# Performance work log

Measured on AMD Instinct MI355X. Metric: run time of the kernel, lower is better.

## Reference

```python
import jax, jax.numpy as jnp
import numpy as np

N = 12288
E = 393216
IN_DIM = 128
HID = 64
QK = 32
K_HOPS = 2


def setup_inputs() -> dict:
    key = jax.random.key(0)
    ks = jax.random.split(key, 12)
    s = lambda k, shp, fan: jax.random.normal(k, shp, jnp.float32) / np.sqrt(fan)
    return {
        "x_train": jax.random.normal(ks[0], (N, IN_DIM), jnp.float32),
        "x_ori": jax.random.normal(ks[1], (N, IN_DIM), jnp.float32),
        "edge_index": jax.random.randint(ks[2], (2, E), 0, N, jnp.int64),
        "mask": jnp.zeros((N,), jnp.bool_),
        "W1": s(ks[3], (IN_DIM, HID), IN_DIM), "b1": jnp.zeros((HID,), jnp.float32),
        "W2": s(ks[4], (HID, HID), HID),      "b2": jnp.zeros((HID,), jnp.float32),
        "Wq": s(ks[5], (HID, QK), HID),       "bq": jnp.zeros((QK,), jnp.float32),
        "Wk": s(ks[6], (HID, QK), HID),       "bk": jnp.zeros((QK,), jnp.float32),
        "Wv": s(ks[7], (HID, HID), HID),      "bv": jnp.zeros((HID,), jnp.float32),
        "Wdx": s(ks[8], (HID, IN_DIM), HID),  "bdx": jnp.zeros((IN_DIM,), jnp.float32),
    }


def reference(x_train, x_ori, edge_index, mask,
              W1, b1, W2, b2, Wq, bq, Wk, bk, Wv, bv, Wdx, bdx):
    n = x_train.shape[0]
    row, col = edge_index[0], edge_index[1]

    # shared MLP: linear -> relu -> linear2 -> relu
    enc = lambda x: jax.nn.relu(jax.nn.relu(x @ W1 + b1) @ W2 + b2)
    h_ori = enc(x_ori)      # [N, HID]
    h_train = enc(x_train)  # [N, HID]

    # degree of source nodes, D^{-1/2}
    deg = jax.ops.segment_sum(jnp.ones_like(row, jnp.float32), row, num_segments=n)
    d_invsqrt = jnp.clip(deg, 1.0, None) ** -0.5  # [N]
    d_invsqrt = d_invsqrt[:, None]

    def lap(x):
        h = x * d_invsqrt
        out = jax.ops.segment_sum(h[row], col, num_segments=n)
        return x - out * d_invsqrt

    a_feat = 2.0 * h_train - lap(h_train)  # low-pass: 2I - L_sym
    stack = [a_feat]
    x = h_train
    for _ in range(K_HOPS):  # dropout inert in eval mode
        x = lap(x)
        stack.append(x)
    L = jnp.stack(stack, axis=1)  # [N, K+1, HID]

    # attention with global mean-pooled query over h_ori[~mask]
    w = (~mask).astype(jnp.float32)
    q_nodes = h_ori @ Wq + bq                              # [N, QK]
    q_global = (q_nodes * w[:, None]).sum(0) / jnp.clip(w.sum(), 1.0, None)  # [QK]
    keys = L @ Wk + bk   # [N, K+1, QK]
    vals = L @ Wv + bv   # [N, K+1, HID]
    scale = 1.0 / np.sqrt(HID)  # scale uses D = keys feature dim BEFORE projection
    scores = jnp.einsum('q,nkq->nk', q_global, keys) * scale
    A = jax.nn.softmax(scores, axis=-1)          # [N, K+1]
    z = jnp.einsum('nk,nkd->nd', A, vals)        # [N, HID]

    x_hat = z @ Wdx + bdx   # [N, IN_DIM]
    adj_hat = z @ z.T       # [N, N]
    return x_hat, adj_hat
```

## Files before the change

### kernel.cpp

```cpp
#include <hip/hip_runtime.h>
#include <hip/hip_bf16.h>

constexpr int N_  = 12288;
constexpr int E_  = 393216;
constexpr int IND = 128;
constexpr int HID = 64;
constexpr int QKD = 32;
constexpr int CAP = 96;

typedef __attribute__((ext_vector_type(4))) float f4raw;
typedef __attribute__((ext_vector_type(8))) __bf16 bf16x8;
typedef __attribute__((ext_vector_type(4))) __bf16 bf16x4;
typedef __attribute__((ext_vector_type(16))) float f32x16;

__device__ inline bf16x8 lds_read_bf8(const char* base, int row, int k) {
  int off = (row * 128 + k * 2) ^ ((row & 7) << 4);
  uint4 u = *(const uint4*)(base + off);
  union { uint4 u; bf16x8 v; } c; c.u = u; return c.v;
}
__device__ inline void lds_write_bf(char* base, int row, int col, __bf16 v) {
  int off = (row * 128 + col * 2) ^ ((row & 7) << 4);
  *(__bf16*)(base + off) = v;
}

__global__ __launch_bounds__(256) void prep_graph_kernel(
    const float* __restrict__ xo, const float* __restrict__ xt,
    const int* __restrict__ row, const int* __restrict__ col,
    const float* __restrict__ W1, const float* __restrict__ W2,
    const float* __restrict__ Wv, const float* __restrict__ Wdx,
    __bf16* __restrict__ xb, __bf16* __restrict__ W1T, __bf16* __restrict__ W2T,
    __bf16* __restrict__ WvT, __bf16* __restrict__ WdxT,
    int* degRow, int* cntCol, int* __restrict__ csrRow) {
  int b = blockIdx.x, tid = threadIdx.x;
  if (b < 384) {
    int e0 = (b * 256 + tid) * 4;
    int4 r4 = *(const int4*)(row + e0);
    atomicAdd(&degRow[r4.x], 1);
    atomicAdd(&degRow[r4.y], 1);
    atomicAdd(&degRow[r4.z], 1);
    atomicAdd(&degRow[r4.w], 1);
  } else if (b < 768) {
    int e0 = ((b - 384) * 256 + tid) * 4;
    int4 r4 = *(const int4*)(row + e0);
    int4 c4 = *(const int4*)(col + e0);
    int p;
    p = atomicAdd(&cntCol[c4.x], 1); csrRow[c4.x * CAP + p] = r4.x;
    p = atomicAdd(&cntCol[c4.y], 1); csrRow[c4.y * CAP + p] = r4.y;
    p = atomicAdd(&cntCol[c4.z], 1); csrRow[c4.z * CAP + p] = r4.z;
    p = atomicAdd(&cntCol[c4.w], 1); csrRow[c4.w * CAP + p] = r4.w;
  } else if (b < 2304) {
    size_t base = (size_t)(b - 768) * 2048 + (size_t)tid * 8;
    const size_t half = (size_t)N_ * IND;
    const float* src = (base < half) ? (xo + base) : (xt + (base - half));
    f4raw v0 = *(const f4raw*)(src);
    f4raw v1 = *(const f4raw*)(src + 4);
    bf16x8 o;
    o[0] = (__bf16)v0.x; o[1] = (__bf16)v0.y; o[2] = (__bf16)v0.z; o[3] = (__bf16)v0.w;
    o[4] = (__bf16)v1.x; o[5] = (__bf16)v1.y; o[6] = (__bf16)v1.z; o[7] = (__bf16)v1.w;
    *(bf16x8*)(xb + base) = o;
  } else if (b == 2304) {
    for (int e = tid; e < IND * HID; e += 256) {
      int c = e >> 7, k = e & 127;
      W1T[e] = (__bf16)W1[k * HID + c];
    }
  } else if (b == 2305) {
    for (int e = tid; e < HID * HID; e += 256) {
      int c = e >> 6, k = e & 63;
      W2T[e] = (__bf16)W2[k * HID + c];
    }
  } else if (b == 2306) {
    for (int e = tid; e < HID * HID; e += 256) {
      int c = e >> 6, k = e & 63;
      WvT[e] = (__bf16)Wv[k * HID + c];
    }
  } else {
    for (int e = tid; e < HID * IND; e += 256) {
      int c = e >> 6, k = e & 63;
      WdxT[e] = (__bf16)Wdx[k * IND + c];
    }
  }
}

__global__ __launch_bounds__(256) void enc_dinv_kernel(
    const __bf16* __restrict__ xb,
    const __bf16* __restrict__ W1T, const float* __restrict__ b1,
    const __bf16* __restrict__ W2T, const float* __restrict__ b2,
    const int* __restrict__ degRow, const unsigned char* __restrict__ mask,
    float* __restrict__ h_tr, float* __restrict__ dinv, float* __restrict__ gsum) {
  __shared__ __align__(16) char h1s[2][32 * 128];
  __shared__ float wls[64];
  int b = blockIdx.x, tid = threadIdx.x;
  if (b >= 384) {
    int i0 = ((b - 384) * 256 + tid) * 4;
    int4 dg = *(const int4*)(degRow + i0);
    f4raw o = {rsqrtf((float)max(dg.x, 1)), rsqrtf((float)max(dg.y, 1)),
               rsqrtf((float)max(dg.z, 1)), rsqrtf((float)max(dg.w, 1))};
    *(f4raw*)(dinv + i0) = o;
    return;
  }
  bool ori = b < 192;
  int row0 = (ori ? b : b - 192) * 64;
  const __bf16* xrow = xb + (ori ? (size_t)0 : (size_t)N_ * IND) + (size_t)row0 * IND;
  if (ori && tid < 64) wls[tid] = mask[row0 + tid] ? 0.f : 1.f;
  int wave = tid >> 6, lane = tid & 63;
  int p = wave >> 1, w2 = wave & 1;
  int lr = lane & 31, hi = lane >> 5;
  int colc = w2 * 32 + lr;
  f32x16 acc = (f32x16)(0.f);
  const __bf16* wcol = W1T + (size_t)colc * IND + hi * 8;
  const __bf16* arow = xrow + (size_t)(p * 32 + lr) * IND + hi * 8;
#pragma unroll
  for (int kk = 0; kk < 8; ++kk) {
    bf16x8 a = *(const bf16x8*)(arow + kk * 16);
    bf16x8 bq = *(const bf16x8*)(wcol + kk * 16);
    acc = __builtin_amdgcn_mfma_f32_32x32x16_bf16(a, bq, acc, 0, 0, 0);
  }
  float b1l = b1[colc];
#pragma unroll
  for (int reg = 0; reg < 16; ++reg) {
    int rr = (reg & 3) + 8 * (reg >> 2) + 4 * hi;
    float v = fmaxf(acc[reg] + b1l, 0.f);
    lds_write_bf(h1s[p], rr, colc, (__bf16)v);
  }
  __syncthreads();
  f32x16 acc2 = (f32x16)(0.f);
  const __bf16* wcol2 = W2T + (size_t)colc * HID + hi * 8;
#pragma unroll
  for (int kk = 0; kk < 4; ++kk) {
    bf16x8 a = lds_read_bf8(h1s[p], lr, kk * 16 + hi * 8);
    bf16x8 bq = *(const bf16x8*)(wcol2 + kk * 16);
    acc2 = __builtin_amdgcn_mfma_f32_32x32x16_bf16(a, bq, acc2, 0, 0, 0);
  }
  float b2l = b2[colc];
  if (ori) {
    float part = 0.f;
#pragma unroll
    for (int reg = 0; reg < 16; ++reg) {
      int rr = (reg & 3) + 8 * (reg >> 2) + 4 * hi;
      float v = fmaxf(acc2[reg] + b2l, 0.f);
      part = fmaf(wls[p * 32 + rr], v, part);
    }
    atomicAdd(&gsum[colc], part);
    if (tid == 0) {
      float wl = 0.f;
      for (int r = 0; r < 64; ++r) wl += wls[r];
      atomicAdd(&gsum[64], wl);
    }
  } else {
#pragma unroll
    for (int reg = 0; reg < 16; ++reg) {
      int rr = (reg & 3) + 8 * (reg >> 2) + 4 * hi;
      float v = fmaxf(acc2[reg] + b2l, 0.f);
      h_tr[(size_t)(row0 + p * 32 + rr) * HID + colc] = v;
    }
  }
}

__global__ __launch_bounds__(256) void lap1_kernel(
    const float* __restrict__ h, const float* __restrict__ dinv,
    const int* __restrict__ cnt, const int* __restrict__ csrRow,
    float* __restrict__ lap1d) {
  int lane = threadIdx.x & 63, wv = threadIdx.x >> 6;
  int g = lane >> 4, t = lane & 15;
  int c = blockIdx.x * 16 + wv * 4 + g;
  int s0 = c * CAP, s1 = s0 + cnt[c];
  f4raw a0 = (f4raw)(0.f), a1 = (f4raw)(0.f);
  int i = s0;
  for (; i + 1 < s1; i += 2) {
    int r0 = csrRow[i], r1 = csrRow[i + 1];
    a0 += (*(const f4raw*)(h + (size_t)r0 * HID + t * 4)) * dinv[r0];
    a1 += (*(const f4raw*)(h + (size_t)r1 * HID + t * 4)) * dinv[r1];
  }
  if (i < s1) {
    int r0 = csrRow[i];
    a0 += (*(const f4raw*)(h + (size_t)r0 * HID + t * 4)) * dinv[r0];
  }
  float d = dinv[c];
  size_t idx = (size_t)c * HID + t * 4;
  f4raw hc = *(const f4raw*)(h + idx);
  *(f4raw*)(lap1d + idx) = (hc - (a0 + a1) * d) * d;
}

__global__ __launch_bounds__(256) void lap2_attnz_xhat_kernel(
    const float* __restrict__ h, const float* __restrict__ lap1d,
    const float* __restrict__ dinv,
    const int* __restrict__ cnt, const int* __restrict__ csrRow,
    const float* __restrict__ gsum,
    const float* __restrict__ Wq, const float* __restrict__ bq,
    const float* __restrict__ Wk, const float* __restrict__ bk,
    const __bf16* __restrict__ WvT, const float* __restrict__ bv,
    const __bf16* __restrict__ WdxT, const float* __restrict__ bdx,
    float* __restrict__ xhat, __bf16* __restrict__ zb) {
  __shared__ float l2s[32][68];
  __shared__ __align__(16) char zps[32 * 128];
  __shared__ __align__(16) char zsl[32 * 128];
  __shared__ float qg[QKD];
  __shared__ float kqs[72];
  int tid = threadIdx.x;
  int row0 = blockIdx.x * 32;
  float wsum = gsum[64];
  if (tid < QKD) {
    float inv = 1.0f / fmaxf(wsum, 1.0f);
    float a = bq[tid] * wsum;
    for (int d0 = 0; d0 < HID; ++d0) a = fmaf(gsum[d0], Wq[d0 * QKD + tid], a);
    qg[tid] = a * inv;
  }
  int grp = tid >> 4, t = tid & 15;
#pragma unroll
  for (int it = 0; it < 2; ++it) {
    int r = grp + 16 * it;
    int c = row0 + r;
    int s0 = c * CAP, s1 = s0 + cnt[c];
    f4raw a0 = (f4raw)(0.f), a1 = (f4raw)(0.f);
    int i = s0;
    for (; i + 1 < s1; i += 2) {
      int r0 = csrRow[i], r1 = csrRow[i + 1];
      a0 += *(const f4raw*)(lap1d + (size_t)r0 * HID + t * 4);
      a1 += *(const f4raw*)(lap1d + (size_t)r1 * HID + t * 4);
    }
    if (i < s1) {
      int r0 = csrRow[i];
      a0 += *(const f4raw*)(lap1d + (size_t)r0 * HID + t * 4);
    }
    float d = dinv[c];
    float rd = 1.0f / d;
    f4raw lv = *(const f4raw*)(lap1d + (size_t)c * HID + t * 4);
    *(f4raw*)&l2s[r][t * 4] = lv * rd - (a0 + a1) * d;
  }
  __syncthreads();
  if (tid < 64) {
    float a = 0.f;
    for (int q = 0; q < QKD; ++q) a = fmaf(Wk[tid * QKD + q], qg[q], a);
    kqs[tid] = a * 0.125f;
  } else if (tid == 64) {
    float sb = 0.f;
    for (int q = 0; q < QKD; ++q) sb = fmaf(bk[q], qg[q], sb);
    kqs[64] = sb * 0.125f;
  }
  __syncthreads();
  f4raw kq4 = *(const f4raw*)(&kqs[t * 4]);
  float sbias = kqs[64];
#pragma unroll
  for (int it = 0; it < 2; ++it) {
    int r = grp + 16 * it;
    int c = row0 + r;
    size_t idx = (size_t)c * HID + t * 4;
    float d = dinv[c];
    float rd = 1.0f / d;
    f4raw hv = *(const f4raw*)(h + idx);
    f4raw v1 = *(const f4raw*)(lap1d + idx) * rd;
    f4raw v2 = *(const f4raw*)&l2s[r][t * 4];
    f4raw av = 2.f * hv - v1;
    float s0 = av.x * kq4.x + av.y * kq4.y + av.z * kq4.z + av.w * kq4.w;
    float s1 = v1.x * kq4.x + v1.y * kq4.y + v1.z * kq4.z + v1.w * kq4.w;
    float s2 = v2.x * kq4.x + v2.y * kq4.y + v2.z * kq4.z + v2.w * kq4.w;
#pragma unroll
    for (int o = 1; o < 16; o <<= 1) {
      s0 += __shfl_xor(s0, o);
      s1 += __shfl_xor(s1, o);
      s2 += __shfl_xor(s2, o);
    }
    s0 += sbias; s1 += sbias; s2 += sbias;
    float m = fmaxf(s0, fmaxf(s1, s2));
    float e0 = __expf(s0 - m), e1 = __expf(s1 - m), e2 = __expf(s2 - m);
    float is = 1.f / (e0 + e1 + e2);
    f4raw zp = (e0 * av + e1 * v1 + e2 * v2) * is;
    bf16x4 z4;
    z4[0] = (__bf16)zp.x; z4[1] = (__bf16)zp.y; z4[2] = (__bf16)zp.z; z4[3] = (__bf16)zp.w;
    int off = (r * 128 + t * 8) ^ ((r & 7) << 4);
    *(bf16x4*)(zps + off) = z4;
  }
  __syncthreads();
  int wave = tid >> 6, lane = tid & 63;
  int lr = lane & 31, hi = lane >> 5;
  if (wave < 2) {
    int col = wave * 32 + lr;
    f32x16 accz = (f32x16)(0.f);
    const __bf16* wv = WvT + (size_t)col * HID + hi * 8;
#pragma unroll
    for (int kk = 0; kk < 4; ++kk) {
      bf16x8 a = lds_read_bf8(zps, lr, kk * 16 + hi * 8);
      bf16x8 bq = *(const bf16x8*)(wv + kk * 16);
      accz = __builtin_amdgcn_mfma_f32_32x32x16_bf16(a, bq, accz, 0, 0, 0);
    }
    float bvl = bv[col];
#pragma unroll
    for (int reg = 0; reg < 16; ++reg) {
      int rr = (reg & 3) + 8 * (reg >> 2) + 4 * hi;
      __bf16 vb = (__bf16)(accz[reg] + bvl);
      zb[(size_t)(row0 + rr) * HID + col] = vb;
      lds_write_bf(zsl, rr, col, vb);
    }
  }
  __syncthreads();
  {
    int c0 = wave * 32 + lr;
    f32x16 acx = (f32x16)(0.f);
    const __bf16* wd = WdxT + (size_t)c0 * HID + hi * 8;
#pragma unroll
    for (int kk = 0; kk < 4; ++kk) {
      bf16x8 a = lds_read_bf8(zsl, lr, kk * 16 + hi * 8);
      bf16x8 bq = *(const bf16x8*)(wd + kk * 16);
      acx = __builtin_amdgcn_mfma_f32_32x32x16_bf16(a, bq, acx, 0, 0, 0);
    }
    float bdl = bdx[c0];
#pragma unroll
    for (int reg = 0; reg < 16; ++reg) {
      int rr = (reg & 3) + 8 * (reg >> 2) + 4 * hi;
      xhat[(size_t)(row0 + rr) * IND + c0] = acx[reg] + bdl;
    }
  }
}

__global__ __launch_bounds__(256) void adj_mfma_kernel(
    const __bf16* __restrict__ z, float* __restrict__ out) {
  int tid = threadIdx.x;
  int wave = tid >> 6, lane = tid & 63;
  int wr = wave >> 1, wc = wave & 1;
  int rb = blockIdx.y, cb = blockIdx.x;
  int lr = lane & 31, hi = lane >> 5;

  size_t arow0 = (size_t)(rb * 128 + wr * 64 + lr) * HID;
  size_t arow1 = arow0 + (size_t)32 * HID;
  size_t brow0 = (size_t)(cb * 128 + wc * 64 + lr) * HID;
  size_t brow1 = brow0 + (size_t)32 * HID;
  int kbase = hi * 8;

  f32x16 acc00 = (f32x16)(0.f), acc01 = (f32x16)(0.f);
  f32x16 acc10 = (f32x16)(0.f), acc11 = (f32x16)(0.f);

#pragma unroll
  for (int kk = 0; kk < 4; ++kk) {
    int k0 = kk * 16 + kbase;
    bf16x8 a0 = *(const bf16x8*)(z + arow0 + k0);
    bf16x8 a1 = *(const bf16x8*)(z + arow1 + k0);
    bf16x8 b0 = *(const bf16x8*)(z + brow0 + k0);
    bf16x8 b1 = *(const bf16x8*)(z + brow1 + k0);
    acc00 = __builtin_amdgcn_mfma_f32_32x32x16_bf16(a0, b0, acc00, 0, 0, 0);
    acc01 = __builtin_amdgcn_mfma_f32_32x32x16_bf16(a0, b1, acc01, 0, 0, 0);
    acc10 = __builtin_amdgcn_mfma_f32_32x32x16_bf16(a1, b0, acc10, 0, 0, 0);
    acc11 = __builtin_amdgcn_mfma_f32_32x32x16_bf16(a1, b1, acc11, 0, 0, 0);
  }

  int colb = cb * 128 + wc * 64 + lr;
  int rowb = rb * 128 + wr * 64 + 4 * hi;
#pragma unroll
  for (int reg = 0; reg < 16; ++reg) {
    int rr = (reg & 3) + 8 * (reg >> 2);
    size_t r0 = (size_t)(rowb + rr);
    __builtin_nontemporal_store(acc00[reg], out + r0 * N_ + colb);
    __builtin_nontemporal_store(acc01[reg], out + r0 * N_ + colb + 32);
    __builtin_nontemporal_store(acc10[reg], out + (r0 + 32) * N_ + colb);
    __builtin_nontemporal_store(acc11[reg], out + (r0 + 32) * N_ + colb + 32);
  }
}

extern "C" void kernel_launch(void* const* d_in, const int* in_sizes, int n_in,
                              void* d_out, int out_size, void* d_ws, size_t ws_size,
                              hipStream_t stream) {
  const float* x_train = (const float*)d_in[0];
  const float* x_ori   = (const float*)d_in[1];
  const int*   ei      = (const int*)d_in[2];
  const unsigned char* mask = (const unsigned char*)d_in[3];
  const float* W1  = (const float*)d_in[4];
  const float* b1  = (const float*)d_in[5];
  const float* W2  = (const float*)d_in[6];
  const float* b2  = (const float*)d_in[7];
  const float* Wq  = (const float*)d_in[8];
  const float* bq  = (const float*)d_in[9];
  const float* Wk  = (const float*)d_in[10];
  const float* bk  = (const float*)d_in[11];
  const float* Wv  = (const float*)d_in[12];
  const float* bv  = (const float*)d_in[13];
  const float* Wdx = (const float*)d_in[14];
  const float* bdx = (const float*)d_in[15];

  char* ws = (char*)d_ws;
  size_t o = 0;
  auto alloc = [&](size_t bytes) -> void* {
    void* p = ws + o;
    o += (bytes + 255) & ~(size_t)255;
    return p;
  };
  __bf16* xb    = (__bf16*)alloc((size_t)2 * N_ * IND * 2);
  __bf16* W1T   = (__bf16*)alloc((size_t)IND * HID * 2);
  __bf16* W2T   = (__bf16*)alloc((size_t)HID * HID * 2);
  __bf16* WvT   = (__bf16*)alloc((size_t)HID * HID * 2);
  __bf16* WdxT  = (__bf16*)alloc((size_t)HID * IND * 2);
  float* h_tr   = (float*)alloc((size_t)N_ * HID * 4);
  float* lap1d  = (float*)alloc((size_t)N_ * HID * 4);
  __bf16* zb    = (__bf16*)alloc((size_t)N_ * HID * 2);
  float* dinv   = (float*)alloc((size_t)N_ * 4);
  int*   csrRow = (int*)alloc((size_t)N_ * CAP * 4);
  int*   zero0  = (int*)alloc((size_t)(2 * N_ + 65) * 4);
  int*   degRow = zero0;
  int*   cntCol = zero0 + N_;
  float* gsum   = (float*)(zero0 + 2 * N_);

  const int* row = ei;
  const int* col = ei + E_;

  (void)hipMemsetAsync(zero0, 0, (size_t)(2 * N_ + 65) * 4, stream);

  prep_graph_kernel<<<2308, 256, 0, stream>>>(x_ori, x_train, row, col,
                                              W1, W2, Wv, Wdx,
                                              xb, W1T, W2T, WvT, WdxT,
                                              degRow, cntCol, csrRow);
  enc_dinv_kernel<<<396, 256, 0, stream>>>(xb, W1T, b1, W2T, b2, degRow, mask,
                                           h_tr, dinv, gsum);
  lap1_kernel<<<N_ / 16, 256, 0, stream>>>(h_tr, dinv, cntCol, csrRow, lap1d);

  float* outp = (float*)d_out;
  lap2_attnz_xhat_kernel<<<N_ / 32, 256, 0, stream>>>(h_tr, lap1d, dinv,
                                                      cntCol, csrRow, gsum,
                                                      Wq, bq, Wk, bk, WvT, bv,
                                                      WdxT, bdx, outp, zb);
  adj_mfma_kernel<<<dim3(96, 96), 256, 0, stream>>>(zb, outp + (size_t)N_ * IND);
}
```

Measured before the change: 254.2 us.

## Fold Wv into Wdx so x_hat runs in parallel with z projection

Precomputes the combined weight Wv·Wdx and bias bv·Wdx+bdx in the prep kernel. x_hat can then be computed directly from the attention-pooled features, on waves 2-3, at the same time as waves 0-1 compute z. This removes a serial MFMA stage, an LDS buffer and a barrier from the fused kernel. It also unrolls the CSR gather loops in both Laplacian kernels to four accumulators for more memory-level parallelism. The fused weight is rounded to bf16 once, which changes rounding slightly, and the 8192-element weight product runs serially on a single prep block.

```diff
diff --git a/kernel.cpp b/kernel.cpp
--- a/kernel.cpp
+++ b/kernel.cpp
@@ -28,8 +28,9 @@
     const int* __restrict__ row, const int* __restrict__ col,
     const float* __restrict__ W1, const float* __restrict__ W2,
     const float* __restrict__ Wv, const float* __restrict__ Wdx,
+    const float* __restrict__ bv, const float* __restrict__ bdx,
     __bf16* __restrict__ xb, __bf16* __restrict__ W1T, __bf16* __restrict__ W2T,
-    __bf16* __restrict__ WvT, __bf16* __restrict__ WdxT,
+    __bf16* __restrict__ WvT, __bf16* __restrict__ WvdxT, float* __restrict__ bvdx,
     int* degRow, int* cntCol, int* __restrict__ csrRow) {
   int b = blockIdx.x, tid = threadIdx.x;
   if (b < 384) {
@@ -74,9 +75,16 @@
       WvT[e] = (__bf16)Wv[k * HID + c];
     }
   } else {
-    for (int e = tid; e < HID * IND; e += 256) {
+    for (int e = tid; e < IND * HID; e += 256) {
       int c = e >> 6, k = e & 63;
-      WdxT[e] = (__bf16)Wdx[k * IND + c];
+      float a = 0.f;
+      for (int j = 0; j < HID; ++j) a = fmaf(Wv[k * HID + j], Wdx[j * IND + c], a);
+      WvdxT[e] = (__bf16)a;
+    }
+    if (tid < IND) {
+      float a = bdx[tid];
+      for (int j = 0; j < HID; ++j) a = fmaf(bv[j], Wdx[j * IND + tid], a);
+      bvdx[tid] = a;
     }
   }
 }
@@ -164,21 +172,23 @@
   int g = lane >> 4, t = lane & 15;
   int c = blockIdx.x * 16 + wv * 4 + g;
   int s0 = c * CAP, s1 = s0 + cnt[c];
-  f4raw a0 = (f4raw)(0.f), a1 = (f4raw)(0.f);
+  f4raw a0 = (f4raw)(0.f), a1 = (f4raw)(0.f), a2 = (f4raw)(0.f), a3 = (f4raw)(0.f);
   int i = s0;
-  for (; i + 1 < s1; i += 2) {
-    int r0 = csrRow[i], r1 = csrRow[i + 1];
+  for (; i + 3 < s1; i += 4) {
+    int r0 = csrRow[i], r1 = csrRow[i + 1], r2 = csrRow[i + 2], r3 = csrRow[i + 3];
     a0 += (*(const f4raw*)(h + (size_t)r0 * HID + t * 4)) * dinv[r0];
     a1 += (*(const f4raw*)(h + (size_t)r1 * HID + t * 4)) * dinv[r1];
-  }
-  if (i < s1) {
+    a2 += (*(const f4raw*)(h + (size_t)r2 * HID + t * 4)) * dinv[r2];
+    a3 += (*(const f4raw*)(h + (size_t)r3 * HID + t * 4)) * dinv[r3];
+  }
+  for (; i < s1; ++i) {
     int r0 = csrRow[i];
     a0 += (*(const f4raw*)(h + (size_t)r0 * HID + t * 4)) * dinv[r0];
   }
   float d = dinv[c];
   size_t idx = (size_t)c * HID + t * 4;
   f4raw hc = *(const f4raw*)(h + idx);
-  *(f4raw*)(lap1d + idx) = (hc - (a0 + a1) * d) * d;
+  *(f4raw*)(lap1d + idx) = (hc - ((a0 + a1) + (a2 + a3)) * d) * d;
 }
 
 __global__ __launch_bounds__(256) void lap2_attnz_xhat_kernel(
@@ -189,11 +199,10 @@
     const float* __restrict__ Wq, const float* __restrict__ bq,
     const float* __restrict__ Wk, const float* __restrict__ bk,
     const __bf16* __restrict__ WvT, const float* __restrict__ bv,
-    const __bf16* __restrict__ WdxT, const float* __restrict__ bdx,
+    const __bf16* __restrict__ WvdxT, const float* __restrict__ bvdx,
     float* __restrict__ xhat, __bf16* __restrict__ zb) {
   __shared__ float l2s[32][68];
   __shared__ __align__(16) char zps[32 * 128];
-  __shared__ __align__(16) char zsl[32 * 128];
   __shared__ float qg[QKD];
   __shared__ float kqs[72];
   int tid = threadIdx.x;
@@ -211,21 +220,23 @@
     int r = grp + 16 * it;
     int c = row0 + r;
     int s0 = c * CAP, s1 = s0 + cnt[c];
-    f4raw a0 = (f4raw)(0.f), a1 = (f4raw)(0.f);
+    f4raw a0 = (f4raw)(0.f), a1 = (f4raw)(0.f), a2 = (f4raw)(0.f), a3 = (f4raw)(0.f);
     int i = s0;
-    for (; i + 1 < s1; i += 2) {
-      int r0 = csrRow[i], r1 = csrRow[i + 1];
+    for (; i + 3 < s1; i += 4) {
+      int r0 = csrRow[i], r1 = csrRow[i + 1], r2 = csrRow[i + 2], r3 = csrRow[i + 3];
       a0 += *(const f4raw*)(lap1d + (size_t)r0 * HID + t * 4);
       a1 += *(const f4raw*)(lap1d + (size_t)r1 * HID + t * 4);
-    }
-    if (i < s1) {
+      a2 += *(const f4raw*)(lap1d + (size_t)r2 * HID + t * 4);
+      a3 += *(const f4raw*)(lap1d + (size_t)r3 * HID + t * 4);
+    }
+    for (; i < s1; ++i) {
       int r0 = csrRow[i];
       a0 += *(const f4raw*)(lap1d + (size_t)r0 * HID + t * 4);
     }
     float d = dinv[c];
     float rd = 1.0f / d;
     f4raw lv = *(const f4raw*)(lap1d + (size_t)c * HID + t * 4);
-    *(f4raw*)&l2s[r][t * 4] = lv * rd - (a0 + a1) * d;
+    *(f4raw*)&l2s[r][t * 4] = lv * rd - ((a0 + a1) + (a2 + a3)) * d;
   }
   __syncthreads();
   if (tid < 64) {
@@ -287,27 +298,27 @@
 #pragma unroll
     for (int reg = 0; reg < 16; ++reg) {
       int rr = (reg & 3) + 8 * (reg >> 2) + 4 * hi;
-      __bf16 vb = (__bf16)(accz[reg] + bvl);
-      zb[(size_t)(row0 + rr) * HID + col] = vb;
-      lds_write_bf(zsl, rr, col, vb);
-    }
-  }
-  __syncthreads();
-  {
-    int c0 = wave * 32 + lr;
-    f32x16 acx = (f32x16)(0.f);
-    const __bf16* wd = WdxT + (size_t)c0 * HID + hi * 8;
-#pragma unroll
-    for (int kk = 0; kk < 4; ++kk) {
-      bf16x8 a = lds_read_bf8(zsl, lr, kk * 16 + hi * 8);
-      bf16x8 bq = *(const bf16x8*)(wd + kk * 16);
-      acx = __builtin_amdgcn_mfma_f32_32x32x16_bf16(a, bq, acx, 0, 0, 0);
-    }
-    float bdl = bdx[c0];
-#pragma unroll
-    for (int reg = 0; reg < 16; ++reg) {
-      int rr = (reg & 3) + 8 * (reg >> 2) + 4 * hi;
-      xhat[(size_t)(row0 + rr) * IND + c0] = acx[reg] + bdl;
+      zb[(size_t)(row0 + rr) * HID + col] = (__bf16)(accz[reg] + bvl);
+    }
+  } else {
+    int w2 = wave - 2;
+#pragma unroll
+    for (int tt = 0; tt < 2; ++tt) {
+      int c0 = w2 * 32 + tt * 64 + lr;
+      f32x16 acx = (f32x16)(0.f);
+      const __bf16* wd = WvdxT + (size_t)c0 * HID + hi * 8;
+#pragma unroll
+      for (int kk = 0; kk < 4; ++kk) {
+        bf16x8 a = lds_read_bf8(zps, lr, kk * 16 + hi * 8);
+        bf16x8 bq = *(const bf16x8*)(wd + kk * 16);
+        acx = __builtin_amdgcn_mfma_f32_32x32x16_bf16(a, bq, acx, 0, 0, 0);
+      }
+      float bdl = bvdx[c0];
+#pragma unroll
+      for (int reg = 0; reg < 16; ++reg) {
+        int rr = (reg & 3) + 8 * (reg >> 2) + 4 * hi;
+        xhat[(size_t)(row0 + rr) * IND + c0] = acx[reg] + bdl;
+      }
     }
   }
 }
@@ -386,7 +397,8 @@
   __bf16* W1T   = (__bf16*)alloc((size_t)IND * HID * 2);
   __bf16* W2T   = (__bf16*)alloc((size_t)HID * HID * 2);
   __bf16* WvT   = (__bf16*)alloc((size_t)HID * HID * 2);
-  __bf16* WdxT  = (__bf16*)alloc((size_t)HID * IND * 2);
+  __bf16* WvdxT = (__bf16*)alloc((size_t)HID * IND * 2);
+  float* bvdx   = (float*)alloc((size_t)IND * 4);
   float* h_tr   = (float*)alloc((size_t)N_ * HID * 4);
   float* lap1d  = (float*)alloc((size_t)N_ * HID * 4);
   __bf16* zb    = (__bf16*)alloc((size_t)N_ * HID * 2);
@@ -403,8 +415,8 @@
   (void)hipMemsetAsync(zero0, 0, (size_t)(2 * N_ + 65) * 4, stream);
 
   prep_graph_kernel<<<2308, 256, 0, stream>>>(x_ori, x_train, row, col,
-                                              W1, W2, Wv, Wdx,
-                                              xb, W1T, W2T, WvT, WdxT,
+                                              W1, W2, Wv, Wdx, bv, bdx,
+                                              xb, W1T, W2T, WvT, WvdxT, bvdx,
                                               degRow, cntCol, csrRow);
   enc_dinv_kernel<<<396, 256, 0, stream>>>(xb, W1T, b1, W2T, b2, degRow, mask,
                                            h_tr, dinv, gsum);
@@ -414,6 +426,6 @@
   lap2_attnz_xhat_kernel<<<N_ / 32, 256, 0, stream>>>(h_tr, lap1d, dinv,
                                                       cntCol, csrRow, gsum,
                                                       Wq, bq, Wk, bk, WvT, bv,
-                                                      WdxT, bdx, outp, zb);
+                                                      WvdxT, bvdx, outp, zb);
   adj_mfma_kernel<<<dim3(96, 96), 256, 0, stream>>>(zb, outp + (size_t)N_ * IND);
 }
```

Measured after the change: 314.0 us. 1.24x slower.
